# Kernel tuning notes

Hardware: AMD Instinct MI355X
Metric: run time of the kernel (lower is better)

Reference implementation:

```python
import jax, jax.numpy as jnp
import numpy as np

N_GROUPS = 32
EPS = 1e-5
N_HEADS = 8
D_K = 64


def setup_inputs() -> dict:
    key = jax.random.key(0)
    ks = jax.random.split(key, 4)
    B, C, H, W = 16, 512, 32, 32
    x = jax.random.normal(ks[0], (B, C, H, W), dtype=jnp.float32)
    gn_w = jnp.ones((C,), dtype=jnp.float32)
    gn_b = jnp.zeros((C,), dtype=jnp.float32)
    proj_w = jax.random.normal(ks[1], (3 * C, C), dtype=jnp.float32) * (C ** -0.5)
    proj_b = jnp.zeros((3 * C,), dtype=jnp.float32)
    out_w = jax.random.normal(ks[2], (C, C), dtype=jnp.float32) * (C ** -0.5)
    out_b = jnp.zeros((C,), dtype=jnp.float32)
    return {"x": x, "gn_w": gn_w, "gn_b": gn_b, "proj_w": proj_w,
            "proj_b": proj_b, "out_w": out_w, "out_b": out_b}


def _group_norm(x, w, b):
    B, C, H, W = x.shape
    xg = x.reshape(B, N_GROUPS, C // N_GROUPS, H, W)
    mean = xg.mean(axis=(2, 3, 4), keepdims=True)
    var = xg.var(axis=(2, 3, 4), keepdims=True)
    xn = (xg - mean) * jax.lax.rsqrt(var + EPS)
    xn = xn.reshape(B, C, H, W)
    return xn * w[None, :, None, None] + b[None, :, None, None]


def reference(x, gn_w, gn_b, proj_w, proj_b, out_w, out_b):
    B, C, H, W = x.shape
    S = H * W
    scale = D_K ** -0.25  # applied to both q and k, as in the original
    h = _group_norm(x, gn_w, gn_b).reshape(B, C, S).transpose(0, 2, 1)  # [B,S,C]
    qkv = h @ proj_w.T + proj_b  # [B,S,3C]
    qkv = qkv.reshape(B, S, N_HEADS, 3 * D_K)
    q, k, v = jnp.split(qkv, 3, axis=-1)  # each [B,S,H,D]
    attn = jnp.einsum('bihd,bjhd->bijh', q * scale, k * scale)  # [B,S,S,Hd]
    attn = jax.nn.softmax(attn, axis=2)
    res = jnp.einsum('bijh,bjhd->bihd', attn, v).reshape(B, S, N_HEADS * D_K)
    res = res @ out_w.T + out_b  # [B,S,C]
    res = res.transpose(0, 2, 1).reshape(B, C, H, W)
    return res + x
```

## Files before the change

### kernel.cpp

```cpp
#include <hip/hip_runtime.h>
#include <stdint.h>

typedef unsigned short u16;
typedef __attribute__((ext_vector_type(8))) short bf16x8;
typedef __attribute__((ext_vector_type(4))) short bf16x4;
typedef __attribute__((ext_vector_type(4))) float f32x4;
typedef __attribute__((ext_vector_type(4))) unsigned short u16x4;

#define GLD16(gp, lp) __builtin_amdgcn_global_load_lds( \
    (__attribute__((address_space(1))) void*)(void*)(gp), \
    (__attribute__((address_space(3))) void*)(void*)(lp), 16, 0, 0)

__device__ __forceinline__ u16 f2b(float f) {
  union { float f; unsigned u; } v; v.f = f;
  unsigned r = v.u + 0x7FFFu + ((v.u >> 16) & 1u);
  return (u16)(r >> 16);
}

__global__ __launch_bounds__(256) void cvt_kernel(const float* __restrict__ w,
                                                  u16* __restrict__ o, int n4) {
  int i = blockIdx.x * 256 + threadIdx.x;
  if (i < n4) {
    const float4 f = ((const float4*)w)[i];
    u16x4 r; r[0] = f2b(f.x); r[1] = f2b(f.y); r[2] = f2b(f.z); r[3] = f2b(f.w);
    *(u16x4*)(o + (size_t)i * 4) = r;
  }
}

__global__ __launch_bounds__(256) void gn_kernel(const float* __restrict__ x,
                                                 const float* __restrict__ gw,
                                                 const float* __restrict__ gb,
                                                 u16* __restrict__ h) {
  const int b = blockIdx.x >> 5, g = blockIdx.x & 31;
  const float* xg = x + ((size_t)(b * 512 + g * 16)) * 1024;
  const int tid = threadIdx.x;
  float vals[64];
  float s = 0.f, ss = 0.f;
#pragma unroll
  for (int i = 0; i < 64; i++) {
    float vv = xg[i * 256 + tid];
    vals[i] = vv; s += vv; ss += vv * vv;
  }
#pragma unroll
  for (int off = 32; off; off >>= 1) { s += __shfl_down(s, off); ss += __shfl_down(ss, off); }
  __shared__ float red[8];
  const int wid = tid >> 6, lane = tid & 63;
  if (lane == 0) { red[wid] = s; red[4 + wid] = ss; }
  __syncthreads();
  if (tid == 0) {
    float S = red[0] + red[1] + red[2] + red[3];
    float SS = red[4] + red[5] + red[6] + red[7];
    float mean = S * (1.f / 16384.f);
    float var = SS * (1.f / 16384.f) - mean * mean;
    red[0] = mean; red[1] = rsqrtf(var + 1e-5f);
  }
  __syncthreads();
  const float mean = red[0], rs = red[1];
  float sc[16], bi[16];
#pragma unroll
  for (int c = 0; c < 16; c++) { sc[c] = gw[g * 16 + c] * rs; bi[c] = gb[g * 16 + c]; }
#pragma unroll
  for (int h4 = 0; h4 < 4; h4++) {
    const int sp = h4 * 256 + tid;
    u16 row[16];
#pragma unroll
    for (int c = 0; c < 16; c++)
      row[c] = f2b((vals[c * 4 + h4] - mean) * sc[c] + bi[c]);
    u16* dst = h + ((size_t)(b * 1024 + sp)) * 512 + g * 16;
    *(bf16x8*)dst = *(bf16x8*)&row[0];
    *(bf16x8*)(dst + 8) = *(bf16x8*)&row[8];
  }
}

__global__ __launch_bounds__(256) void qkv_gemm(const u16* __restrict__ h,
                                                const u16* __restrict__ w,
                                                const float* __restrict__ bias,
                                                u16* __restrict__ q,
                                                u16* __restrict__ k,
                                                u16* __restrict__ v) {
  __shared__ u16 As[128 * 32];
  __shared__ u16 Bs[128 * 32];
  const int b = blockIdx.z;
  const int bm = blockIdx.x;
  const int bn = blockIdx.y;
  const int tid = threadIdx.x, lane = tid & 63, wid = tid >> 6;
  const int wm = wid & 1, wn = wid >> 1;
  const u16* gA = h + ((size_t)b * 1024 + bm * 128) * 512;
  const u16* gB = w + (size_t)bn * 128 * 512;

  const f32x4 fz = {0.f, 0.f, 0.f, 0.f};
  f32x4 acc[4][4];
#pragma unroll
  for (int i = 0; i < 4; i++)
#pragma unroll
    for (int j = 0; j < 4; j++) acc[i][j] = fz;

  const int r0 = lane >> 2;
  const int ch8 = (lane & 3) * 8;

  for (int kt = 0; kt < 16; ++kt) {
    __syncthreads();
#pragma unroll
    for (int j = 0; j < 2; ++j) {
      const int idx = wid * 2 + j;
      const int row = idx * 16 + r0;
      GLD16(gA + (size_t)row * 512 + kt * 32 + ch8, &As[idx * 512 + lane * 8]);
      GLD16(gB + (size_t)row * 512 + kt * 32 + ch8, &Bs[idx * 512 + lane * 8]);
    }
    __syncthreads();
    bf16x8 af[4], bf[4];
#pragma unroll
    for (int mi = 0; mi < 4; mi++)
      af[mi] = *(const bf16x8*)&As[(wm * 64 + mi * 16 + (lane & 15)) * 32 + (lane >> 4) * 8];
#pragma unroll
    for (int ni = 0; ni < 4; ni++)
      bf[ni] = *(const bf16x8*)&Bs[(wn * 64 + ni * 16 + (lane & 15)) * 32 + (lane >> 4) * 8];
#pragma unroll
    for (int mi = 0; mi < 4; mi++)
#pragma unroll
      for (int ni = 0; ni < 4; ni++)
        acc[mi][ni] = __builtin_amdgcn_mfma_f32_16x16x32_bf16(af[mi], bf[ni], acc[mi][ni], 0, 0, 0);
  }

  const float scale = 0.35355339059327373f;
  const int quad4 = (lane >> 4) << 2;
#pragma unroll
  for (int mi = 0; mi < 4; mi++) {
    const int m = bm * 128 + wm * 64 + mi * 16 + quad4;
#pragma unroll
    for (int ni = 0; ni < 4; ni++) {
      const int n = bn * 128 + wn * 64 + ni * 16 + (lane & 15);
      const int head = n / 192;
      const int rr = n - head * 192;
      const float bi = bias[n];
      const int d = rr & 63;
      if (rr < 128) {
        u16* dst = (rr < 64) ? q : k;
        dst += ((size_t)(b * 8 + head) * 1024 + m) * 64 + d;
#pragma unroll
        for (int r = 0; r < 4; r++)
          dst[(size_t)r * 64] = f2b((acc[mi][ni][r] + bi) * scale);
      } else {
        u16x4 pk;
#pragma unroll
        for (int r = 0; r < 4; r++) pk[r] = f2b(acc[mi][ni][r] + bi);
        *(u16x4*)(v + ((size_t)(b * 8 + head) * 64 + d) * 1024 + m) = pk;
      }
    }
  }
}

__global__ __launch_bounds__(256) void attn_kernel(const u16* __restrict__ q,
                                                   const u16* __restrict__ k,
                                                   const u16* __restrict__ vT,
                                                   u16* __restrict__ o) {
  __shared__ u16 Ks[64 * 72];
  __shared__ u16 Vs[64 * 72];
  const int bh = blockIdx.x;
  const int qb = blockIdx.y;
  const int tid = threadIdx.x, lane = tid & 63, wid = tid >> 6;
  const u16* Q = q + (size_t)bh * 1024 * 64;
  const u16* K = k + (size_t)bh * 1024 * 64;
  const u16* V = vT + (size_t)bh * 64 * 1024;
  const int qrow0 = qb * 128 + wid * 32;
  const int c15 = lane & 15, quad = lane >> 4;
  const int srow = tid >> 2;
  const int scol = (tid & 3) * 16;
  const int ldsrow = srow * 72 + scol;

  bf16x8 qf[2][2];
#pragma unroll
  for (int kk = 0; kk < 2; kk++)
#pragma unroll
    for (int ni = 0; ni < 2; ni++)
      qf[kk][ni] = *(const bf16x8*)(Q + (size_t)(qrow0 + ni * 16 + c15) * 64 + kk * 32 + quad * 8);

  const f32x4 fz = {0.f, 0.f, 0.f, 0.f};
  const float Mshift = 10.f;
  const f32x4 fm = {-Mshift, -Mshift, -Mshift, -Mshift};
  f32x4 oaccT[4][2];
#pragma unroll
  for (int i = 0; i < 4; i++)
#pragma unroll
    for (int j = 0; j < 2; j++) oaccT[i][j] = fz;
  float lsum[2] = {0.f, 0.f};

  bf16x8 kr0, kr1, vr0, vr1;
  {
    const u16* Kn = K + (size_t)srow * 64 + scol;
    kr0 = *(const bf16x8*)(Kn); kr1 = *(const bf16x8*)(Kn + 8);
    const u16* Vn = V + (size_t)srow * 1024 + scol;
    vr0 = *(const bf16x8*)(Vn); vr1 = *(const bf16x8*)(Vn + 8);
  }

  for (int kt = 0; kt < 16; ++kt) {
    __syncthreads();
    *(bf16x8*)&Ks[ldsrow] = kr0; *(bf16x8*)&Ks[ldsrow + 8] = kr1;
    *(bf16x8*)&Vs[ldsrow] = vr0; *(bf16x8*)&Vs[ldsrow + 8] = vr1;
    __syncthreads();
    const int nk = (kt + 1) & 15;
    {
      const u16* Kn = K + ((size_t)nk * 64 + srow) * 64 + scol;
      kr0 = *(const bf16x8*)(Kn); kr1 = *(const bf16x8*)(Kn + 8);
      const u16* Vn = V + (size_t)srow * 1024 + nk * 64 + scol;
      vr0 = *(const bf16x8*)(Vn); vr1 = *(const bf16x8*)(Vn + 8);
    }

    f32x4 sacc[4][2];
#pragma unroll
    for (int i = 0; i < 4; i++)
#pragma unroll
      for (int j = 0; j < 2; j++) sacc[i][j] = fm;
#pragma unroll
    for (int kk = 0; kk < 2; kk++) {
      bf16x8 af[4];
#pragma unroll
      for (int mi = 0; mi < 4; mi++)
        af[mi] = *(const bf16x8*)&Ks[(mi * 16 + c15) * 72 + kk * 32 + quad * 8];
#pragma unroll
      for (int mi = 0; mi < 4; mi++)
#pragma unroll
        for (int ni = 0; ni < 2; ni++)
          sacc[mi][ni] = __builtin_amdgcn_mfma_f32_16x16x32_bf16(af[mi], qf[kk][ni], sacc[mi][ni], 0, 0, 0);
    }

    unsigned pkd[4][2][2];
#pragma unroll
    for (int ni = 0; ni < 2; ni++) {
      float ls = 0.f;
#pragma unroll
      for (int mi = 0; mi < 4; mi++) {
        unsigned pu[4];
#pragma unroll
        for (int r = 0; r < 4; r++) {
          const float p = __expf(sacc[mi][ni][r]);
          ls += p;
          union { float f; unsigned u; } c; c.f = p;
          pu[r] = c.u + 0x8000u;
        }
        pkd[mi][ni][0] = __builtin_amdgcn_perm(pu[1], pu[0], 0x07060302u);
        pkd[mi][ni][1] = __builtin_amdgcn_perm(pu[3], pu[2], 0x07060302u);
      }
      lsum[ni] += ls;
    }

#pragma unroll
    for (int mg = 0; mg < 2; mg++) {
      union { unsigned u[4]; bf16x8 v; } bb[2];
#pragma unroll
      for (int ni = 0; ni < 2; ni++) {
        bb[ni].u[0] = pkd[2 * mg][ni][0];     bb[ni].u[1] = pkd[2 * mg][ni][1];
        bb[ni].u[2] = pkd[2 * mg + 1][ni][0]; bb[ni].u[3] = pkd[2 * mg + 1][ni][1];
      }
#pragma unroll
      for (int nd = 0; nd < 4; nd++) {
        union { bf16x4 h[2]; bf16x8 v; } aa;
        const int vbase = (nd * 16 + c15) * 72 + mg * 32 + quad * 4;
        aa.h[0] = *(const bf16x4*)&Vs[vbase];
        aa.h[1] = *(const bf16x4*)&Vs[vbase + 16];
#pragma unroll
        for (int ni = 0; ni < 2; ni++)
          oaccT[nd][ni] = __builtin_amdgcn_mfma_f32_16x16x32_bf16(aa.v, bb[ni].v, oaccT[nd][ni], 0, 0, 0);
      }
    }
  }

  float iv[2];
#pragma unroll
  for (int ni = 0; ni < 2; ni++) {
    float l = lsum[ni];
    l += __shfl_xor(l, 16);
    l += __shfl_xor(l, 32);
    iv[ni] = 1.f / l;
  }
  const int b = bh >> 3, hh = bh & 7;
#pragma unroll
  for (int ni = 0; ni < 2; ni++) {
    const int row = qrow0 + ni * 16 + c15;
#pragma unroll
    for (int nd = 0; nd < 4; nd++) {
      u16x4 pk4;
#pragma unroll
      for (int r = 0; r < 4; r++) pk4[r] = f2b(oaccT[nd][ni][r] * iv[ni]);
      *(u16x4*)(o + ((size_t)b * 1024 + row) * 512 + hh * 64 + nd * 16 + quad * 4) = pk4;
    }
  }
}

__global__ __launch_bounds__(256) void out_gemm(const u16* __restrict__ wo,
                                                const u16* __restrict__ attn,
                                                const float* __restrict__ ob,
                                                const float* __restrict__ x,
                                                float* __restrict__ out) {
  __shared__ u16 As[128 * 32];
  __shared__ u16 Bs[128 * 32];
  const int b = blockIdx.z;
  const int bm = blockIdx.x;
  const int bn = blockIdx.y;
  const int tid = threadIdx.x, lane = tid & 63, wid = tid >> 6;
  const int wm = wid & 1, wn = wid >> 1;
  const u16* gA = wo + (size_t)bm * 128 * 512;
  const u16* gB = attn + ((size_t)b * 1024 + bn * 128) * 512;

  const f32x4 fz = {0.f, 0.f, 0.f, 0.f};
  f32x4 acc[4][4];
#pragma unroll
  for (int i = 0; i < 4; i++)
#pragma unroll
    for (int j = 0; j < 4; j++) acc[i][j] = fz;

  const int r0 = lane >> 2;
  const int ch8 = (lane & 3) * 8;

  for (int kt = 0; kt < 16; ++kt) {
    __syncthreads();
#pragma unroll
    for (int j = 0; j < 2; ++j) {
      const int idx = wid * 2 + j;
      const int row = idx * 16 + r0;
      GLD16(gA + (size_t)row * 512 + kt * 32 + ch8, &As[idx * 512 + lane * 8]);
      GLD16(gB + (size_t)row * 512 + kt * 32 + ch8, &Bs[idx * 512 + lane * 8]);
    }
    __syncthreads();
    bf16x8 af[4], bf[4];
#pragma unroll
    for (int mi = 0; mi < 4; mi++)
      af[mi] = *(const bf16x8*)&As[(wm * 64 + mi * 16 + (lane & 15)) * 32 + (lane >> 4) * 8];
#pragma unroll
    for (int ni = 0; ni < 4; ni++)
      bf[ni] = *(const bf16x8*)&Bs[(wn * 64 + ni * 16 + (lane & 15)) * 32 + (lane >> 4) * 8];
#pragma unroll
    for (int mi = 0; mi < 4; mi++)
#pragma unroll
      for (int ni = 0; ni < 4; ni++)
        acc[mi][ni] = __builtin_amdgcn_mfma_f32_16x16x32_bf16(af[mi], bf[ni], acc[mi][ni], 0, 0, 0);
  }

  const int quad4 = (lane >> 4) << 2;
#pragma unroll
  for (int mi = 0; mi < 4; mi++) {
    const int c = bm * 128 + wm * 64 + mi * 16 + quad4;
#pragma unroll
    for (int ni = 0; ni < 4; ni++) {
      const int s = bn * 128 + wn * 64 + ni * 16 + (lane & 15);
#pragma unroll
      for (int r = 0; r < 4; r++) {
        const int cc = c + r;
        const size_t idx = ((size_t)b * 512 + cc) * 1024 + s;
        out[idx] = acc[mi][ni][r] + ob[cc] + x[idx];
      }
    }
  }
}

extern "C" void kernel_launch(void* const* d_in, const int* in_sizes, int n_in,
                              void* d_out, int out_size, void* d_ws, size_t ws_size,
                              hipStream_t stream) {
  const float* x      = (const float*)d_in[0];
  const float* gn_w   = (const float*)d_in[1];
  const float* gn_b   = (const float*)d_in[2];
  const float* proj_w = (const float*)d_in[3];
  const float* proj_b = (const float*)d_in[4];
  const float* out_w  = (const float*)d_in[5];
  const float* out_b  = (const float*)d_in[6];
  float* out = (float*)d_out;

  char* p = (char*)d_ws;
  u16* h    = (u16*)p; p += (size_t)16 * 1024 * 512 * 2;
  u16* q    = (u16*)p; p += (size_t)16 * 8 * 1024 * 64 * 2;
  u16* k    = (u16*)p; p += (size_t)16 * 8 * 1024 * 64 * 2;
  u16* v    = (u16*)p; p += (size_t)16 * 8 * 1024 * 64 * 2;
  u16* attn = (u16*)p; p += (size_t)16 * 1024 * 512 * 2;
  u16* wq   = (u16*)p; p += (size_t)1536 * 512 * 2;
  u16* wo   = (u16*)p; p += (size_t)512 * 512 * 2;

  cvt_kernel<<<768, 256, 0, stream>>>(proj_w, wq, 196608);
  cvt_kernel<<<256, 256, 0, stream>>>(out_w, wo, 65536);
  gn_kernel<<<512, 256, 0, stream>>>(x, gn_w, gn_b, h);
  qkv_gemm<<<dim3(8, 12, 16), 256, 0, stream>>>(h, wq, proj_b, q, k, v);
  attn_kernel<<<dim3(128, 8, 1), 256, 0, stream>>>(q, k, v, attn);
  out_gemm<<<dim3(4, 8, 16), 256, 0, stream>>>(wo, attn, out_b, x, out);
}
```

Baseline: 223.2 us.

## Swizzle attention LDS tiles and fold log2e into q scale for exp2

Replaces the padded K/V shared-memory tiles (row stride 72) with unpadded 64-wide tiles using an XOR swizzle. The V tile is stored pre-permuted so each MFMA operand becomes a single 16-byte LDS read instead of two 8-byte reads. It also multiplies log2(e) into the q scale, raises the fixed softmax shift to match, and calls the hardware exp2 directly to drop the multiply inside __expf. In exchange the LDS write pattern for V gets more complex (four 8-byte stores) and correctness now depends on the swizzle indices matching between writes and reads.

```diff
diff --git a/kernel.cpp b/kernel.cpp
--- a/kernel.cpp
+++ b/kernel.cpp
@@ -15,6 +15,14 @@
   union { float f; unsigned u; } v; v.f = f;
   unsigned r = v.u + 0x7FFFu + ((v.u >> 16) & 1u);
   return (u16)(r >> 16);
+}
+
+__device__ __forceinline__ float fexp2(float x) {
+#if __has_builtin(__builtin_amdgcn_exp2f)
+  return __builtin_amdgcn_exp2f(x);
+#else
+  return exp2f(x);
+#endif
 }
 
 __global__ __launch_bounds__(256) void cvt_kernel(const float* __restrict__ w,
@@ -122,7 +130,8 @@
         acc[mi][ni] = __builtin_amdgcn_mfma_f32_16x16x32_bf16(af[mi], bf[ni], acc[mi][ni], 0, 0, 0);
   }
 
-  const float scale = 0.35355339059327373f;
+  const float qscale = 0.51006972f;
+  const float kscale = 0.35355339059327373f;
   const int quad4 = (lane >> 4) << 2;
 #pragma unroll
   for (int mi = 0; mi < 4; mi++) {
@@ -136,10 +145,11 @@
       const int d = rr & 63;
       if (rr < 128) {
         u16* dst = (rr < 64) ? q : k;
+        const float sc = (rr < 64) ? qscale : kscale;
         dst += ((size_t)(b * 8 + head) * 1024 + m) * 64 + d;
 #pragma unroll
         for (int r = 0; r < 4; r++)
-          dst[(size_t)r * 64] = f2b((acc[mi][ni][r] + bi) * scale);
+          dst[(size_t)r * 64] = f2b((acc[mi][ni][r] + bi) * sc);
       } else {
         u16x4 pk;
 #pragma unroll
@@ -154,8 +164,8 @@
                                                    const u16* __restrict__ k,
                                                    const u16* __restrict__ vT,
                                                    u16* __restrict__ o) {
-  __shared__ u16 Ks[64 * 72];
-  __shared__ u16 Vs[64 * 72];
+  __shared__ u16 Ks[64 * 64];
+  __shared__ u16 Vs[64 * 64];
   const int bh = blockIdx.x;
   const int qb = blockIdx.y;
   const int tid = threadIdx.x, lane = tid & 63, wid = tid >> 6;
@@ -164,9 +174,16 @@
   const u16* V = vT + (size_t)bh * 64 * 1024;
   const int qrow0 = qb * 128 + wid * 32;
   const int c15 = lane & 15, quad = lane >> 4;
+  const int sw = c15 & 7;
   const int srow = tid >> 2;
-  const int scol = (tid & 3) * 16;
-  const int ldsrow = srow * 72 + scol;
+  const int t4 = tid & 3;
+  const int s7 = srow & 7;
+  const int kld0 = srow * 64 + (((t4 * 2) ^ s7) * 8);
+  const int kld1 = srow * 64 + (((t4 * 2 + 1) ^ s7) * 8);
+  int vld[4];
+#pragma unroll
+  for (int qq = 0; qq < 4; qq++)
+    vld[qq] = srow * 64 + ((((t4 >> 1) * 4 + qq) ^ s7) * 8) + (t4 & 1) * 4;
 
   bf16x8 qf[2][2];
 #pragma unroll
@@ -176,7 +193,7 @@
       qf[kk][ni] = *(const bf16x8*)(Q + (size_t)(qrow0 + ni * 16 + c15) * 64 + kk * 32 + quad * 8);
 
   const f32x4 fz = {0.f, 0.f, 0.f, 0.f};
-  const float Mshift = 10.f;
+  const float Mshift = 14.4269504089f;
   const f32x4 fm = {-Mshift, -Mshift, -Mshift, -Mshift};
   f32x4 oaccT[4][2];
 #pragma unroll
@@ -187,22 +204,29 @@
 
   bf16x8 kr0, kr1, vr0, vr1;
   {
-    const u16* Kn = K + (size_t)srow * 64 + scol;
+    const u16* Kn = K + (size_t)srow * 64 + t4 * 16;
     kr0 = *(const bf16x8*)(Kn); kr1 = *(const bf16x8*)(Kn + 8);
-    const u16* Vn = V + (size_t)srow * 1024 + scol;
+    const u16* Vn = V + (size_t)srow * 1024 + t4 * 16;
     vr0 = *(const bf16x8*)(Vn); vr1 = *(const bf16x8*)(Vn + 8);
   }
 
   for (int kt = 0; kt < 16; ++kt) {
     __syncthreads();
-    *(bf16x8*)&Ks[ldsrow] = kr0; *(bf16x8*)&Ks[ldsrow + 8] = kr1;
-    *(bf16x8*)&Vs[ldsrow] = vr0; *(bf16x8*)&Vs[ldsrow + 8] = vr1;
+    *(bf16x8*)&Ks[kld0] = kr0; *(bf16x8*)&Ks[kld1] = kr1;
+    {
+      union { bf16x4 h[2]; bf16x8 v; } a0, a1;
+      a0.v = vr0; a1.v = vr1;
+      *(bf16x4*)&Vs[vld[0]] = a0.h[0];
+      *(bf16x4*)&Vs[vld[1]] = a0.h[1];
+      *(bf16x4*)&Vs[vld[2]] = a1.h[0];
+      *(bf16x4*)&Vs[vld[3]] = a1.h[1];
+    }
     __syncthreads();
     const int nk = (kt + 1) & 15;
     {
-      const u16* Kn = K + ((size_t)nk * 64 + srow) * 64 + scol;
+      const u16* Kn = K + ((size_t)nk * 64 + srow) * 64 + t4 * 16;
       kr0 = *(const bf16x8*)(Kn); kr1 = *(const bf16x8*)(Kn + 8);
-      const u16* Vn = V + (size_t)srow * 1024 + nk * 64 + scol;
+      const u16* Vn = V + (size_t)srow * 1024 + nk * 64 + t4 * 16;
       vr0 = *(const bf16x8*)(Vn); vr1 = *(const bf16x8*)(Vn + 8);
     }
 
@@ -216,7 +240,7 @@
       bf16x8 af[4];
 #pragma unroll
       for (int mi = 0; mi < 4; mi++)
-        af[mi] = *(const bf16x8*)&Ks[(mi * 16 + c15) * 72 + kk * 32 + quad * 8];
+        af[mi] = *(const bf16x8*)&Ks[(mi * 16 + c15) * 64 + (((kk * 4 + quad) ^ sw) * 8)];
 #pragma unroll
       for (int mi = 0; mi < 4; mi++)
 #pragma unroll
@@ -233,7 +257,7 @@
         unsigned pu[4];
 #pragma unroll
         for (int r = 0; r < 4; r++) {
-          const float p = __expf(sacc[mi][ni][r]);
+          const float p = fexp2(sacc[mi][ni][r]);
           ls += p;
           union { float f; unsigned u; } c; c.f = p;
           pu[r] = c.u + 0x8000u;
@@ -254,13 +278,10 @@
       }
 #pragma unroll
       for (int nd = 0; nd < 4; nd++) {
-        union { bf16x4 h[2]; bf16x8 v; } aa;
-        const int vbase = (nd * 16 + c15) * 72 + mg * 32 + quad * 4;
-        aa.h[0] = *(const bf16x4*)&Vs[vbase];
-        aa.h[1] = *(const bf16x4*)&Vs[vbase + 16];
+        const bf16x8 aa = *(const bf16x8*)&Vs[(nd * 16 + c15) * 64 + (((mg * 4 + quad) ^ sw) * 8)];
 #pragma unroll
         for (int ni = 0; ni < 2; ni++)
-          oaccT[nd][ni] = __builtin_amdgcn_mfma_f32_16x16x32_bf16(aa.v, bb[ni].v, oaccT[nd][ni], 0, 0, 0);
+          oaccT[nd][ni] = __builtin_amdgcn_mfma_f32_16x16x32_bf16(aa, bb[ni].v, oaccT[nd][ni], 0, 0, 0);
       }
     }
   }
```

After: 217.1 us. 2.7% less time.
